# Optimization experiments

Hardware: AMD Instinct MI355X
Metric: run time of the kernel (lower is better)

Reference implementation:

```python
import jax, jax.numpy as jnp
import numpy as np

B, S, HID = 2, 2048, 2048
NH, NKV, HD = 16, 4, 128
GROUPS = NH // NKV
ROPE_BASE = 10000.0


def setup_inputs() -> dict:
    key = jax.random.key(0)
    ks = jax.random.split(key, 12)

    def w(k, i, o):
        return (jax.random.normal(k, (i, o), jnp.float32) * (i ** -0.5)).astype(jnp.float32)

    return {
        'x_real': jax.random.normal(ks[0], (B, S, HID), jnp.float32),
        'x_imag': jax.random.normal(ks[1], (B, S, HID), jnp.float32),
        'Wq_r': w(ks[2], HID, HID), 'Wq_i': w(ks[3], HID, HID),
        'bq_r': jnp.zeros((HID,), jnp.float32), 'bq_i': jnp.zeros((HID,), jnp.float32),
        'Wk_r': w(ks[4], HID, NKV * HD), 'Wk_i': w(ks[5], HID, NKV * HD),
        'bk_r': jnp.zeros((NKV * HD,), jnp.float32), 'bk_i': jnp.zeros((NKV * HD,), jnp.float32),
        'Wv_r': w(ks[6], HID, NKV * HD), 'Wv_i': w(ks[7], HID, NKV * HD),
        'bv_r': jnp.zeros((NKV * HD,), jnp.float32), 'bv_i': jnp.zeros((NKV * HD,), jnp.float32),
        'Wo_r': w(ks[8], HID, HID), 'Wo_i': w(ks[9], HID, HID),
        'bo_r': jnp.zeros((HID,), jnp.float32), 'bo_i': jnp.zeros((HID,), jnp.float32),
    }


def _clinear(xr, xi, Wr, Wi, br, bi):
    # complex linear: (xr + i*xi) @ (Wr + i*Wi) + (br + i*bi)
    out_r = xr @ Wr - xi @ Wi + br
    out_i = xr @ Wi + xi @ Wr + bi
    return out_r, out_i


def _split_heads(xr, xi, n_heads):
    b, s, _ = xr.shape
    xr = xr.reshape(b, s, n_heads, -1).transpose(0, 2, 1, 3)  # [B,H,S,D]
    xi = xi.reshape(b, s, n_heads, -1).transpose(0, 2, 1, 3)
    return xr, xi


def _rope(xr, xi):
    # complex rotary embedding: multiply (xr + i*xi) by exp(i * pos * inv_freq)
    s, d = xr.shape[-2], xr.shape[-1]
    inv_freq = 1.0 / (ROPE_BASE ** (jnp.arange(0, d, 2, dtype=jnp.float32) / d))
    freqs = jnp.arange(s, dtype=jnp.float32)[:, None] * inv_freq[None, :]  # [S, D/2]
    emb = jnp.concatenate([freqs, freqs], axis=-1)  # [S, D]
    cos, sin = jnp.cos(emb), jnp.sin(emb)
    return xr * cos - xi * sin, xr * sin + xi * cos


def _repeat_kv(xr, xi):
    if GROUPS == 1:
        return xr, xi
    b, hkv, s, d = xr.shape
    xr = jnp.broadcast_to(xr[:, :, None], (b, hkv, GROUPS, s, d)).reshape(b, NH, s, d)
    xi = jnp.broadcast_to(xi[:, :, None], (b, hkv, GROUPS, s, d)).reshape(b, NH, s, d)
    return xr, xi


def reference(x_real, x_imag, Wq_r, Wq_i, bq_r, bq_i, Wk_r, Wk_i, bk_r, bk_i,
              Wv_r, Wv_i, bv_r, bv_i, Wo_r, Wo_i, bo_r, bo_i):
    q_r, q_i = _clinear(x_real, x_imag, Wq_r, Wq_i, bq_r, bq_i)
    k_r, k_i = _clinear(x_real, x_imag, Wk_r, Wk_i, bk_r, bk_i)
    v_r, v_i = _clinear(x_real, x_imag, Wv_r, Wv_i, bv_r, bv_i)

    q_r, q_i = _split_heads(q_r, q_i, NH)
    k_r, k_i = _split_heads(k_r, k_i, NKV)
    v_r, v_i = _split_heads(v_r, v_i, NKV)

    q_r, q_i = _rope(q_r, q_i)
    k_r, k_i = _rope(k_r, k_i)

    k_r, k_i = _repeat_kv(k_r, k_i)
    v_r, v_i = _repeat_kv(v_r, v_i)

    scale = 1.0 / jnp.sqrt(jnp.float32(HD))
    # real part of complex inner product q . conj(k)
    scores = (jnp.einsum('bhqd,bhkd->bhqk', q_r, k_r)
              + jnp.einsum('bhqd,bhkd->bhqk', q_i, k_i)) * scale
    s = scores.shape[-1]
    causal = jnp.tril(jnp.ones((s, s), bool))
    scores = jnp.where(causal, scores, jnp.float32(-1e9))
    attn = jax.nn.softmax(scores, axis=-1)  # [B,H,S,S]

    out_r = jnp.einsum('bhqk,bhkd->bhqd', attn, v_r)
    out_i = jnp.einsum('bhqk,bhkd->bhqd', attn, v_i)

    # merge heads
    b = out_r.shape[0]
    out_r = out_r.transpose(0, 2, 1, 3).reshape(b, s, NH * HD)
    out_i = out_i.transpose(0, 2, 1, 3).reshape(b, s, NH * HD)

    out_r, out_i = _clinear(out_r, out_i, Wo_r, Wo_i, bo_r, bo_i)
    return out_r, out_i, attn
```

## Files before the change

kernel.cpp:

```cpp
#include <hip/hip_runtime.h>
#include <hip/hip_bf16.h>

#define S_LEN 2048
#define HIDDEN 2048
#define NHEAD 16
#define NKVH 4
#define HEADD 128
#define BATCH 2

typedef __attribute__((ext_vector_type(4))) float f32x4;
typedef __attribute__((ext_vector_type(8))) short bf16x8;
typedef __attribute__((ext_vector_type(4))) unsigned short u16x4;

__device__ __forceinline__ unsigned short f2bf(float f) {
  union { __hip_bfloat16 h; unsigned short u; } cv;
  cv.h = __float2bfloat16(f);
  return cv.u;
}

__device__ __forceinline__ float bf2f(unsigned short u) {
  union { float f; unsigned int i; } cv;
  cv.i = (unsigned int)u << 16;
  return cv.f;
}

__device__ __forceinline__ void gl_lds16(const void* g, void* l) {
  __builtin_amdgcn_global_load_lds(
      (const __attribute__((address_space(1))) unsigned int*)g,
      (__attribute__((address_space(3))) unsigned int*)l,
      16, 0, 0);
}

__device__ __forceinline__ f32x4 mfma16(bf16x8 a, bf16x8 b, f32x4 c) {
  return __builtin_amdgcn_mfma_f32_16x16x32_bf16(a, b, c, 0, 0, 0);
}

__global__ void k_rope_table(float* tab) {
  int idx = blockIdx.x * blockDim.x + threadIdx.x;
  if (idx >= S_LEN * 64) return;
  int s = idx >> 6, j = idx & 63;
  float invf = expf(-(float)j * (logf(10000.0f) / 64.0f));
  float ang = (float)s * invf;
  float sn, cs;
  sincosf(ang, &sn, &cs);
  tab[idx * 2 + 0] = cs;
  tab[idx * 2 + 1] = sn;
}

__global__ void k_pack_x(const float* __restrict__ xr, const float* __restrict__ xi,
                         unsigned short* __restrict__ Xp) {
  int idx = blockIdx.x * blockDim.x + threadIdx.x;
  if (idx >= 4096 * 4096 / 4) return;
  int m = idx >> 10;
  int c4 = idx & 1023;
  const float* src = (c4 < 512) ? (xr + (size_t)m * 2048 + c4 * 4)
                                : (xi + (size_t)m * 2048 + (c4 - 512) * 4);
  f32x4 v = *(const f32x4*)src;
  ((u16x4*)Xp)[idx] = (u16x4){f2bf(v.x), f2bf(v.y), f2bf(v.z), f2bf(v.w)};
}

__global__ void k_pack_w(const float* __restrict__ wq_r, const float* __restrict__ wq_i,
                         const float* __restrict__ wk_r, const float* __restrict__ wk_i,
                         const float* __restrict__ wv_r, const float* __restrict__ wv_i,
                         const float* __restrict__ wo_r, const float* __restrict__ wo_i,
                         unsigned short* __restrict__ Wt) {
  __shared__ float tile[32][33];
  int k0 = blockIdx.x * 32;
  int n0 = blockIdx.y * 32;
  int tx = threadIdx.x, ty0 = threadIdx.y;
#pragma unroll
  for (int i = 0; i < 4; ++i) {
    int ty = ty0 + i * 8;
    int k = k0 + ty;
    int n = n0 + tx;
    const float* Wr; const float* Wi; int w, part, j;
    if (n < 4096) {
      Wr = wq_r; Wi = wq_i; w = 2048;
      int h = n >> 8, p = (n >> 7) & 1, d = n & 127;
      part = p; j = h * 128 + d;
    } else if (n < 5120) {
      Wr = wk_r; Wi = wk_i; w = 512;
      int t = n - 4096;
      int kv = t >> 8, p = (t >> 7) & 1, d = t & 127;
      part = p; j = kv * 128 + d;
    } else if (n < 6144) {
      Wr = wv_r; Wi = wv_i; w = 512;
      int t = n - 5120;
      int kv = t >> 8, p = (t >> 7) & 1, d = t & 127;
      part = p; j = kv * 128 + d;
    } else {
      Wr = wo_r; Wi = wo_i; w = 2048;
      int t = n - 6144;
      part = (t >= w); j = part ? (t - w) : t;
    }
    float v;
    if (part == 0) v = (k < 2048) ? Wr[(size_t)k * w + j] : -Wi[(size_t)(k - 2048) * w + j];
    else           v = (k < 2048) ? Wi[(size_t)k * w + j] :  Wr[(size_t)(k - 2048) * w + j];
    tile[ty][tx] = v;
  }
  __syncthreads();
#pragma unroll
  for (int i = 0; i < 4; ++i) {
    int ty = ty0 + i * 8;
    Wt[(size_t)(n0 + ty) * 4096 + k0 + tx] = f2bf(tile[tx][ty]);
  }
}

template <int MODE>
__global__ __launch_bounds__(512, 2) void k_gemm256(
    const unsigned short* __restrict__ A, const unsigned short* __restrict__ Bt,
    int NTN,
    float* __restrict__ outR, float* __restrict__ outI,
    const float* __restrict__ bR, const float* __restrict__ bI,
    const float* __restrict__ tab,
    const float* __restrict__ bqr, const float* __restrict__ bqi,
    const float* __restrict__ bkr, const float* __restrict__ bki,
    const float* __restrict__ bvr, const float* __restrict__ bvi,
    unsigned short* __restrict__ Qcat, unsigned short* __restrict__ Kcat,
    unsigned short* __restrict__ VtP) {
  constexpr int KD = 4096;
  constexpr int Kb = KD * 2;
  constexpr int NT = KD / 64;
  constexpr int NITER = NT / 2;
  __shared__ __align__(16) char smem[131072];
  int tid = threadIdx.x, lane = tid & 63, wid = tid >> 6;
  int wm = wid >> 2, wn = wid & 3;
  int nwg = gridDim.x;
  int bid = blockIdx.x;
  int swz = (bid & 7) * (nwg >> 3) + (bid >> 3);
  int mt = swz / NTN, nt = swz - mt * NTN;
  int m0 = mt * 256, n0 = nt * 256;

  const char* Ab = (const char*)A + (size_t)m0 * Kb;
  const char* Bb = (const char*)Bt + (size_t)n0 * Kb;
  char* L = smem;

  int i0 = tid, i1 = tid + 512;
  int pl0 = (i0 >> 3) * Kb + (((i0 & 7) ^ ((i0 >> 3) & 7)) << 4);
  int pl1 = (i1 >> 3) * Kb + (((i1 & 7) ^ ((i1 >> 3) & 7)) << 4);

  int jx0 = (((lane >> 4)) ^ (lane & 7)) << 4;
  int jx1 = (((lane >> 4) + 4) ^ (lane & 7)) << 4;
  int arow = (wm * 64 + (lane & 15)) * 128;
  int brow = (wn * 32 + (lane & 15)) * 128;

  auto STAGE_A = [&](int buf, int half, int kt) {
    const char* s = Ab + (size_t)half * 128 * Kb + kt * 128;
    char* d = L + buf * 32768 + half * 16384 + (wid << 10);
    gl_lds16(s + pl0, d);
    gl_lds16(s + pl1, d + 8192);
  };
  auto STAGE_B = [&](int buf, int half, int kt) {
    const char* s = Bb + (size_t)half * 128 * Kb + kt * 128;
    char* d = L + 65536 + buf * 32768 + half * 16384 + (wid << 10);
    gl_lds16(s + pl0, d);
    gl_lds16(s + pl1, d + 8192);
  };
  auto LD_A = [&](bf16x8* dst, int buf, int half) {
    const char* base = L + buf * 32768 + half * 16384 + arow;
#pragma unroll
    for (int mf = 0; mf < 4; ++mf) {
      dst[mf * 2 + 0] = *(const bf16x8*)(base + mf * 2048 + jx0);
      dst[mf * 2 + 1] = *(const bf16x8*)(base + mf * 2048 + jx1);
    }
  };
  auto LD_B = [&](bf16x8* dst, int buf, int half) {
    const char* base = L + 65536 + buf * 32768 + half * 16384 + brow;
#pragma unroll
    for (int nf = 0; nf < 2; ++nf) {
      dst[nf * 2 + 0] = *(const bf16x8*)(base + nf * 2048 + jx0);
      dst[nf * 2 + 1] = *(const bf16x8*)(base + nf * 2048 + jx1);
    }
  };

  f32x4 acc[8][4];
  const f32x4 fz = {0.f, 0.f, 0.f, 0.f};
#pragma unroll
  for (int i = 0; i < 8; ++i)
#pragma unroll
    for (int j = 0; j < 4; ++j) acc[i][j] = fz;

  bf16x8 aX[8], aY[8], bX[4], bY[4];

#define BARR() __builtin_amdgcn_s_barrier()
#define WAITV(drain) do { if (drain) asm volatile("s_waitcnt vmcnt(0)" ::: "memory"); \
                          else       asm volatile("s_waitcnt vmcnt(6)" ::: "memory"); } while (0)
#define MMQ(aS, bS, qm, qn) do { \
    __builtin_amdgcn_s_setprio(1); \
    _Pragma("unroll") \
    for (int mf = 0; mf < 4; ++mf) \
      _Pragma("unroll") \
      for (int nf = 0; nf < 2; ++nf) { \
        acc[(qm)*4+mf][(qn)*2+nf] = mfma16(aS[mf*2+0], bS[nf*2+0], acc[(qm)*4+mf][(qn)*2+nf]); \
        acc[(qm)*4+mf][(qn)*2+nf] = mfma16(aS[mf*2+1], bS[nf*2+1], acc[(qm)*4+mf][(qn)*2+nf]); \
      } \
    __builtin_amdgcn_s_setprio(0); \
  } while (0)

  STAGE_A(0, 0, 0);
  STAGE_B(0, 0, 0);
  STAGE_B(0, 1, 0);
  STAGE_A(0, 1, 0);
  STAGE_A(1, 0, 1);
  STAGE_B(1, 0, 1);
  STAGE_B(1, 1, 1);
  asm volatile("s_waitcnt vmcnt(6)" ::: "memory");
  BARR();

  for (int it = 0; it < NITER; ++it) {
    int t1 = 2 * it + 1, t2 = 2 * it + 2, t3 = 2 * it + 3;
    bool nl = (it < NITER - 1);
    LD_A(aX, 0, 0); LD_B(bX, 0, 0);
    STAGE_A(1, 1, t1);
    BARR(); MMQ(aX, bX, 0, 0); BARR();
    LD_B(bY, 0, 1);
    if (nl) STAGE_A(0, 0, t2);
    BARR(); MMQ(aX, bY, 0, 1); BARR();
    LD_A(aY, 0, 1);
    if (nl) STAGE_B(0, 0, t2);
    BARR(); MMQ(aY, bY, 1, 1); BARR();
    if (nl) STAGE_B(0, 1, t2);
    WAITV(!nl); BARR(); MMQ(aY, bX, 1, 0); BARR();
    LD_A(aX, 1, 0); LD_B(bY, 1, 0);
    if (nl) STAGE_A(0, 1, t2);
    BARR(); MMQ(aX, bY, 0, 0); BARR();
    LD_B(bX, 1, 1);
    if (nl) STAGE_A(1, 0, t3);
    BARR(); MMQ(aX, bX, 0, 1); BARR();
    LD_A(aY, 1, 1);
    if (nl) STAGE_B(1, 0, t3);
    BARR(); MMQ(aY, bX, 1, 1); BARR();
    if (nl) STAGE_B(1, 1, t3);
    WAITV(!nl); BARR(); MMQ(aY, bY, 1, 0); BARR();
  }

  int r0 = (lane >> 4) << 2, col0 = lane & 15;

  if (MODE == 1) {
#pragma unroll
    for (int qm = 0; qm < 2; ++qm)
#pragma unroll
      for (int mf = 0; mf < 4; ++mf)
#pragma unroll
        for (int qn = 0; qn < 2; ++qn)
#pragma unroll
          for (int nf = 0; nf < 2; ++nf) {
            f32x4 v = acc[qm * 4 + mf][qn * 2 + nf];
            int rowb = m0 + qm * 128 + wm * 64 + mf * 16 + r0;
            int col = n0 + qn * 128 + wn * 32 + nf * 16 + col0;
#pragma unroll
            for (int r = 0; r < 4; ++r) {
              int row = rowb + r;
              if (col < 2048) outR[(size_t)row * 2048 + col] = v[r] + bR[col];
              else            outI[(size_t)row * 2048 + (col - 2048)] = v[r] + bI[col - 2048];
            }
          }
    return;
  }

  __syncthreads();
  int bidx = m0 >> 11;
  int s0 = m0 & 2047;

  if (n0 < 5120) {
    bool isQ = (n0 < 4096);
    int hh = isQ ? (n0 >> 8) : ((n0 - 4096) >> 8);
    const float* bRp = isQ ? bqr : bkr;
    const float* bIp = isQ ? bqi : bki;
    int jbase = hh * 128;
#pragma unroll
    for (int qm = 0; qm < 2; ++qm)
#pragma unroll
      for (int mf = 0; mf < 4; ++mf)
#pragma unroll
        for (int nf = 0; nf < 2; ++nf) {
          int d = wn * 32 + nf * 16 + col0;
          f32x4 vr = acc[qm * 4 + mf][0 * 2 + nf];
          f32x4 vi = acc[qm * 4 + mf][1 * 2 + nf];
          float br = bRp[jbase + d], bi = bIp[jbase + d];
#pragma unroll
          for (int r = 0; r < 4; ++r) {
            int lrow = qm * 128 + wm * 64 + mf * 16 + r0 + r;
            int s = s0 + lrow;
            float2 cs = *(const float2*)(tab + ((size_t)s * 64 + (d & 63)) * 2);
            float qr = vr[r] + br;
            float qi = vi[r] + bi;
            float orr = qr * cs.x - qi * cs.y;
            float oii = qr * cs.y + qi * cs.x;
            int swz4 = (lrow & 3) << 3;
            int g0 = (d >> 3) ^ swz4;
            int g1 = ((128 + d) >> 3) ^ swz4;
            *(unsigned short*)(L + lrow * 512 + g0 * 16 + (d & 7) * 2) = f2bf(orr);
            *(unsigned short*)(L + lrow * 512 + g1 * 16 + (d & 7) * 2) = f2bf(oii);
          }
        }
    __syncthreads();
    char* dstb = isQ ? (char*)Qcat + ((size_t)(bidx * 16 + hh) * 2048 + s0) * 512
                     : (char*)Kcat + ((size_t)(bidx * 4 + hh) * 2048 + s0) * 512;
#pragma unroll
    for (int i = 0; i < 16; ++i) {
      int cid = tid + 512 * i;
      int row = cid >> 5, c = cid & 31;
      int g = c ^ ((row & 3) << 3);
      *(f32x4*)(dstb + (size_t)row * 512 + c * 16) = *(const f32x4*)(L + row * 512 + g * 16);
    }
  } else {
    int kv = (n0 - 5120) >> 8;
#pragma unroll
    for (int qm = 0; qm < 2; ++qm)
#pragma unroll
      for (int mf = 0; mf < 4; ++mf)
#pragma unroll
        for (int qn = 0; qn < 2; ++qn)
#pragma unroll
          for (int nf = 0; nf < 2; ++nf) {
            int dloc = wn * 32 + nf * 16 + col0;
            int nlocal = qn * 128 + dloc;
            f32x4 v = acc[qm * 4 + mf][qn * 2 + nf];
            float bias = (qn ? bvi : bvr)[kv * 128 + dloc];
#pragma unroll
            for (int r = 0; r < 4; ++r) {
              int lrow = qm * 128 + wm * 64 + mf * 16 + r0 + r;
              int g = (lrow >> 3) ^ (nlocal & 31);
              *(unsigned short*)(L + nlocal * 512 + g * 16 + (lrow & 7) * 2) =
                  f2bf(v[r] + bias);
            }
          }
    __syncthreads();
    char* dstb = (char*)VtP + (size_t)(bidx * 4 + kv) * 256 * 4096 + (size_t)s0 * 2;
#pragma unroll
    for (int i = 0; i < 16; ++i) {
      int cid = tid + 512 * i;
      int n = cid >> 5, c = cid & 31;
      int g = c ^ (n & 31);
      *(f32x4*)(dstb + (size_t)n * 4096 + c * 16) = *(const f32x4*)(L + n * 512 + g * 16);
    }
  }
#undef BARR
#undef WAITV
#undef MMQ
}

__global__ __launch_bounds__(512, 4) void k_attn_fused(
    const unsigned short* __restrict__ Qcat, const unsigned short* __restrict__ Kcat,
    const unsigned short* __restrict__ Vt, float* __restrict__ attn,
    unsigned short* __restrict__ Cpack) {
  __shared__ __align__(16) char smem[74240];
  const float scale = 0.08838834764831845f;
  const float SH = 16.0f;

  int tid = threadIdx.x, lane = tid & 63, wid = tid >> 6;
  int l15 = lane & 15, l4 = lane >> 4;
  int bid = blockIdx.x;
  int qt = 31 - (bid >> 5), bh = bid & 31;
  int b = bh >> 4, h = bh & 15;
  int nt = qt + 1;

  const char* Qb = (const char*)Qcat + (size_t)bh * S_LEN * 512 + (size_t)qt * 64 * 512;
  const char* Kb = (const char*)Kcat + (size_t)(b * NKVH + (h >> 2)) * S_LEN * 512;
  const char* Vb = (const char*)Vt + (size_t)(b * NKVH + (h >> 2)) * 256 * (size_t)S_LEN * 2;
  float* P = attn + (size_t)bh * S_LEN * S_LEN;

  int r5 = tid >> 5, c5 = tid & 31;
  int sw512 = ((c5 ^ (r5 & 7)) << 4);
  int r3 = tid >> 3, c3 = tid & 7;
  int sw128 = ((c3 ^ (r3 & 7)) << 4);
  char* ldst = smem + (wid << 10);

  auto stQ = [&]() {
#pragma unroll
    for (int c = 0; c < 4; ++c)
      gl_lds16(Qb + (size_t)(c * 16 + r5) * 512 + sw512, ldst + c * 8192);
  };
  auto stK = [&](int base, int kv0) {
#pragma unroll
    for (int c = 0; c < 4; ++c)
      gl_lds16(Kb + (size_t)(kv0 + c * 16 + r5) * 512 + sw512, ldst + base + c * 8192);
  };
  auto stV = [&](int kv0) {
#pragma unroll
    for (int c = 0; c < 4; ++c)
      gl_lds16(Vb + (size_t)(c * 64 + r3) * 4096 + kv0 * 2 + sw128,
               ldst + 32768 + c * 8192);
  };

  float* sPart = (float*)(smem + 65536);
  float* sML = (float*)(smem + 73728);

#define BARL() do { asm volatile("s_waitcnt lgkmcnt(0)" ::: "memory"); \
                    __builtin_amdgcn_s_barrier(); } while (0)

  stQ();
  asm volatile("s_waitcnt vmcnt(0)" ::: "memory");
  __builtin_amdgcn_s_barrier();
  bf16x8 q[8];
  {
    int row = (wid >> 1) * 16 + l15;
#pragma unroll
    for (int kf = 0; kf < 8; ++kf)
      q[kf] = *(const bf16x8*)(smem + row * 512 + (((kf * 4 + l4) ^ (row & 7)) << 4));
  }
  BARL();

  auto QKT = [&](f32x4 accs[2], int kbase) {
#pragma unroll
    for (int kf = 0; kf < 8; ++kf) {
      bf16x8 bb[2];
#pragma unroll
      for (int nf = 0; nf < 2; ++nf) {
        int row = (wid & 1) * 32 + nf * 16 + l15;
        bb[nf] = *(const bf16x8*)(smem + kbase + row * 512 +
                                  (((kf * 4 + l4) ^ (row & 7)) << 4));
      }
      accs[0] = mfma16(q[kf], bb[0], accs[0]);
      accs[1] = mfma16(q[kf], bb[1], accs[1]);
    }
  };

  stK(0, 0);
  stK(32768, 64);
  asm volatile("s_waitcnt vmcnt(4)" ::: "memory");
  __builtin_amdgcn_s_barrier();

  float lacc[4] = {0.f, 0.f, 0.f, 0.f};
  for (int t = 0; t < nt; ++t) {
    int kbase = (t & 1) * 32768;
    f32x4 accs[2];
    accs[0] = (f32x4){0.f, 0.f, 0.f, 0.f};
    accs[1] = (f32x4){0.f, 0.f, 0.f, 0.f};
    QKT(accs, kbase);
    BARL();
    if (t + 2 < nt) stK(kbase, (t + 2) * 64);
    int kv0 = t * 64;
#pragma unroll
    for (int r = 0; r < 4; ++r) {
      int lrow = (wid >> 1) * 16 + l4 * 4 + r;
      int grow = qt * 64 + lrow;
      int cA = kv0 + (wid & 1) * 32 + l15;
      float e0 = (cA <= grow) ? __expf(accs[0][r] * scale - SH) : 0.f;
      float e1 = (cA + 16 <= grow) ? __expf(accs[1][r] * scale - SH) : 0.f;
      lacc[r] += e0 + e1;
    }
    if (t + 1 < nt) {
      if (t + 2 < nt) asm volatile("s_waitcnt vmcnt(4)" ::: "memory");
      else            asm volatile("s_waitcnt vmcnt(0)" ::: "memory");
      __builtin_amdgcn_s_barrier();
    }
  }
#pragma unroll
  for (int r = 0; r < 4; ++r) {
#pragma unroll
    for (int o = 1; o < 16; o <<= 1) lacc[r] += __shfl_xor(lacc[r], o);
  }
  if (l15 == 0) {
#pragma unroll
    for (int r = 0; r < 4; ++r) {
      int lrow = (wid >> 1) * 16 + l4 * 4 + r;
      sPart[(wid & 1) * 64 + lrow] = lacc[r];
    }
  }
  BARL();
  if (tid < 64) sML[tid] = 1.0f / (sPart[tid] + sPart[64 + tid]);
  asm volatile("s_waitcnt vmcnt(0) lgkmcnt(0)" ::: "memory");
  __builtin_amdgcn_s_barrier();

  stK(0, 0);
  stV(0);
  asm volatile("s_waitcnt vmcnt(0)" ::: "memory");
  __builtin_amdgcn_s_barrier();

  int wmP = wid >> 2, wnP = wid & 3;
  f32x4 accp[2][4];
#pragma unroll
  for (int i = 0; i < 2; ++i)
#pragma unroll
    for (int j = 0; j < 4; ++j) accp[i][j] = (f32x4){0.f, 0.f, 0.f, 0.f};

  for (int t = 0; t < nt; ++t) {
    bool more = (t + 1 < nt);
    f32x4 accs[2];
    accs[0] = (f32x4){0.f, 0.f, 0.f, 0.f};
    accs[1] = (f32x4){0.f, 0.f, 0.f, 0.f};
    QKT(accs, 0);
    BARL();
    if (more) stK(0, (t + 1) * 64);
    int kv0 = t * 64;
#pragma unroll
    for (int r = 0; r < 4; ++r) {
      int lrow = (wid >> 1) * 16 + l4 * 4 + r;
      int grow = qt * 64 + lrow;
      float mi = sML[lrow];
#pragma unroll
      for (int nf = 0; nf < 2; ++nf) {
        int lcol = (wid & 1) * 32 + nf * 16 + l15;
        int gcol = kv0 + lcol;
        float s = accs[nf][r] * scale;
        float p = (gcol <= grow) ? __expf(s - SH) * mi : 0.f;
        *(unsigned short*)(smem + 65536 + lrow * 128 +
                           (((lcol >> 3) ^ (lrow & 7)) << 4) + (lcol & 7) * 2) = f2bf(p);
      }
    }
    asm volatile("s_waitcnt lgkmcnt(0)" ::: "memory");
    if (more) asm volatile("s_waitcnt vmcnt(4)" ::: "memory");
    else      asm volatile("s_waitcnt vmcnt(0)" ::: "memory");
    __builtin_amdgcn_s_barrier();
#pragma unroll
    for (int p = 0; p < 2; ++p) {
      int idx = tid + 512 * p;
      int row = idx >> 4, c16 = idx & 15;
      int byte = 65536 + row * 128 + (((c16 >> 1) ^ (row & 7)) << 4) + (c16 & 1) * 8;
      u16x4 pv = *(const u16x4*)(smem + byte);
      f32x4 o = {bf2f(pv.x), bf2f(pv.y), bf2f(pv.z), bf2f(pv.w)};
      *(f32x4*)(P + (size_t)(qt * 64 + row) * S_LEN + kv0 + c16 * 4) = o;
    }
    __builtin_amdgcn_s_setprio(1);
#pragma unroll
    for (int ks = 0; ks < 2; ++ks) {
      bf16x8 a[2], bb[4];
#pragma unroll
      for (int mf = 0; mf < 2; ++mf) {
        int row = wmP * 32 + mf * 16 + l15;
        a[mf] = *(const bf16x8*)(smem + 65536 + row * 128 +
                                 (((ks * 4 + l4) ^ (row & 7)) << 4));
      }
#pragma unroll
      for (int nf = 0; nf < 4; ++nf) {
        int n = wnP * 64 + nf * 16 + l15;
        bb[nf] = *(const bf16x8*)(smem + 32768 + n * 128 +
                                  (((ks * 4 + l4) ^ (n & 7)) << 4));
      }
#pragma unroll
      for (int mf = 0; mf < 2; ++mf)
#pragma unroll
        for (int nf = 0; nf < 4; ++nf)
          accp[mf][nf] = mfma16(a[mf], bb[nf], accp[mf][nf]);
    }
    __builtin_amdgcn_s_setprio(0);
    BARL();
    if (more) {
      stV((t + 1) * 64);
      asm volatile("s_waitcnt vmcnt(6)" ::: "memory");
    }
    __builtin_amdgcn_s_barrier();
  }

  {
    int c0 = 64 * (qt + 1);
    const f32x4 z4 = {0.f, 0.f, 0.f, 0.f};
    for (int rr = 0; rr < 8; ++rr) {
      int grow = qt * 64 + wid * 8 + rr;
      for (int c = c0 + lane * 4; c < 2048; c += 256)
        *(f32x4*)(P + (size_t)grow * S_LEN + c) = z4;
    }
  }
  int r0w = l4 * 4;
#pragma unroll
  for (int mf = 0; mf < 2; ++mf)
#pragma unroll
    for (int nf = 0; nf < 4; ++nf) {
      int gmb = qt * 64 + wmP * 32 + mf * 16 + r0w;
      int nn = wnP * 64 + nf * 16 + l15;
      int gcol = (nn < 128) ? (h * 128 + nn) : (2048 + h * 128 + (nn - 128));
#pragma unroll
      for (int r = 0; r < 4; ++r)
        Cpack[(size_t)(b * S_LEN + gmb + r) * 4096 + gcol] = f2bf(accp[mf][nf][r]);
    }
#undef BARL
}

extern "C" void kernel_launch(void* const* d_in, const int* in_sizes, int n_in,
                              void* d_out, int out_size, void* d_ws, size_t ws_size,
                              hipStream_t stream) {
  const float* xr = (const float*)d_in[0];
  const float* xi = (const float*)d_in[1];
  const float* wq_r = (const float*)d_in[2];
  const float* wq_i = (const float*)d_in[3];
  const float* bq_r = (const float*)d_in[4];
  const float* bq_i = (const float*)d_in[5];
  const float* wk_r = (const float*)d_in[6];
  const float* wk_i = (const float*)d_in[7];
  const float* bk_r = (const float*)d_in[8];
  const float* bk_i = (const float*)d_in[9];
  const float* wv_r = (const float*)d_in[10];
  const float* wv_i = (const float*)d_in[11];
  const float* bv_r = (const float*)d_in[12];
  const float* bv_i = (const float*)d_in[13];
  const float* wo_r = (const float*)d_in[14];
  const float* wo_i = (const float*)d_in[15];
  const float* bo_r = (const float*)d_in[16];
  const float* bo_i = (const float*)d_in[17];

  float* out = (float*)d_out;
  float* outR = out;
  float* outI = out + (size_t)BATCH * S_LEN * HIDDEN;
  float* attn = outI + (size_t)BATCH * S_LEN * HIDDEN;

  char* ws = (char*)d_ws;
  size_t off = 0;
  auto alloc = [&](size_t bytes) {
    char* p = ws + off;
    off += (bytes + 255) & ~(size_t)255;
    return p;
  };
  unsigned short* Xp = (unsigned short*)alloc((size_t)4096 * 4096 * 2);
  unsigned short* Wt = (unsigned short*)alloc((size_t)10240 * 4096 * 2);
  float* tab = (float*)alloc((size_t)S_LEN * 64 * 2 * 4);
  unsigned short* Qcat = (unsigned short*)alloc((size_t)BATCH * NHEAD * S_LEN * 256 * 2);
  unsigned short* Kcat = (unsigned short*)alloc((size_t)BATCH * NKVH * S_LEN * 256 * 2);
  unsigned short* Vt = (unsigned short*)alloc((size_t)BATCH * NKVH * 256 * S_LEN * 2);
  unsigned short* Cpack = Xp;

  k_rope_table<<<512, 256, 0, stream>>>(tab);
  k_pack_x<<<16384, 256, 0, stream>>>(xr, xi, Xp);
  k_pack_w<<<dim3(128, 320), dim3(32, 8), 0, stream>>>(wq_r, wq_i, wk_r, wk_i, wv_r, wv_i,
                                                       wo_r, wo_i, Wt);
  k_gemm256<2><<<384, 512, 0, stream>>>(Xp, Wt, 24,
                                        nullptr, nullptr, nullptr, nullptr,
                                        tab, bq_r, bq_i, bk_r, bk_i, bv_r, bv_i,
                                        Qcat, Kcat, Vt);
  k_attn_fused<<<1024, 512, 0, stream>>>(Qcat, Kcat, Vt, attn, Cpack);
  k_gemm256<1><<<256, 512, 0, stream>>>(Cpack, Wt + (size_t)6144 * 4096, 16,
                                        outR, outI, bo_r, bo_i,
                                        nullptr, nullptr, nullptr, nullptr, nullptr,
                                        nullptr, nullptr, nullptr, nullptr, nullptr);
}
```

Before: 724.7 us.

## Load Q/K/V fragments directly from global memory in attention kernel, double-buffer P

Removes the LDS staging of Q, K and V tiles (async global-to-LDS copies plus their waits and barriers) in the fused attention kernel. MFMA operands are now read straight from global memory, relying on the cache for reuse. The P tile is double-buffered in a much smaller LDS allocation, which lets one barrier per iteration go and may raise occupancy. The cost is uncoalesced, redundant global loads per wave and the loss of the explicit prefetch pipelining.

Result: slower. 1.098 ms (+51.5%).

```diff
diff --git a/kernel.cpp b/kernel.cpp
--- a/kernel.cpp
+++ b/kernel.cpp
@@ -345,7 +345,7 @@
     const unsigned short* __restrict__ Qcat, const unsigned short* __restrict__ Kcat,
     const unsigned short* __restrict__ Vt, float* __restrict__ attn,
     unsigned short* __restrict__ Cpack) {
-  __shared__ __align__(16) char smem[74240];
+  __shared__ __align__(16) char smem[17664];
   const float scale = 0.08838834764831845f;
   const float SH = 16.0f;
 
@@ -361,76 +361,38 @@
   const char* Vb = (const char*)Vt + (size_t)(b * NKVH + (h >> 2)) * 256 * (size_t)S_LEN * 2;
   float* P = attn + (size_t)bh * S_LEN * S_LEN;
 
-  int r5 = tid >> 5, c5 = tid & 31;
-  int sw512 = ((c5 ^ (r5 & 7)) << 4);
-  int r3 = tid >> 3, c3 = tid & 7;
-  int sw128 = ((c3 ^ (r3 & 7)) << 4);
-  char* ldst = smem + (wid << 10);
-
-  auto stQ = [&]() {
-#pragma unroll
-    for (int c = 0; c < 4; ++c)
-      gl_lds16(Qb + (size_t)(c * 16 + r5) * 512 + sw512, ldst + c * 8192);
-  };
-  auto stK = [&](int base, int kv0) {
-#pragma unroll
-    for (int c = 0; c < 4; ++c)
-      gl_lds16(Kb + (size_t)(kv0 + c * 16 + r5) * 512 + sw512, ldst + base + c * 8192);
-  };
-  auto stV = [&](int kv0) {
-#pragma unroll
-    for (int c = 0; c < 4; ++c)
-      gl_lds16(Vb + (size_t)(c * 64 + r3) * 4096 + kv0 * 2 + sw128,
-               ldst + 32768 + c * 8192);
-  };
-
-  float* sPart = (float*)(smem + 65536);
-  float* sML = (float*)(smem + 73728);
+  float* sPart = (float*)(smem + 16384);
+  float* sML = (float*)(smem + 16896);
 
 #define BARL() do { asm volatile("s_waitcnt lgkmcnt(0)" ::: "memory"); \
                     __builtin_amdgcn_s_barrier(); } while (0)
 
-  stQ();
-  asm volatile("s_waitcnt vmcnt(0)" ::: "memory");
-  __builtin_amdgcn_s_barrier();
   bf16x8 q[8];
   {
     int row = (wid >> 1) * 16 + l15;
 #pragma unroll
     for (int kf = 0; kf < 8; ++kf)
-      q[kf] = *(const bf16x8*)(smem + row * 512 + (((kf * 4 + l4) ^ (row & 7)) << 4));
-  }
-  BARL();
-
-  auto QKT = [&](f32x4 accs[2], int kbase) {
+      q[kf] = *(const bf16x8*)(Qb + (size_t)row * 512 + (kf * 4 + l4) * 16);
+  }
+
+  int krow0 = (wid & 1) * 32 + l15;
+  auto QKT = [&](f32x4 accs[2], int t) {
+    const char* kb = Kb + (size_t)(t * 64 + krow0) * 512 + l4 * 16;
 #pragma unroll
     for (int kf = 0; kf < 8; ++kf) {
-      bf16x8 bb[2];
-#pragma unroll
-      for (int nf = 0; nf < 2; ++nf) {
-        int row = (wid & 1) * 32 + nf * 16 + l15;
-        bb[nf] = *(const bf16x8*)(smem + kbase + row * 512 +
-                                  (((kf * 4 + l4) ^ (row & 7)) << 4));
-      }
-      accs[0] = mfma16(q[kf], bb[0], accs[0]);
-      accs[1] = mfma16(q[kf], bb[1], accs[1]);
+      bf16x8 b0 = *(const bf16x8*)(kb + kf * 64);
+      bf16x8 b1 = *(const bf16x8*)(kb + 16 * 512 + kf * 64);
+      accs[0] = mfma16(q[kf], b0, accs[0]);
+      accs[1] = mfma16(q[kf], b1, accs[1]);
     }
   };
-
-  stK(0, 0);
-  stK(32768, 64);
-  asm volatile("s_waitcnt vmcnt(4)" ::: "memory");
-  __builtin_amdgcn_s_barrier();
 
   float lacc[4] = {0.f, 0.f, 0.f, 0.f};
   for (int t = 0; t < nt; ++t) {
-    int kbase = (t & 1) * 32768;
     f32x4 accs[2];
     accs[0] = (f32x4){0.f, 0.f, 0.f, 0.f};
     accs[1] = (f32x4){0.f, 0.f, 0.f, 0.f};
-    QKT(accs, kbase);
-    BARL();
-    if (t + 2 < nt) stK(kbase, (t + 2) * 64);
+    QKT(accs, t);
     int kv0 = t * 64;
 #pragma unroll
     for (int r = 0; r < 4; ++r) {
@@ -441,11 +403,6 @@
       float e1 = (cA + 16 <= grow) ? __expf(accs[1][r] * scale - SH) : 0.f;
       lacc[r] += e0 + e1;
     }
-    if (t + 1 < nt) {
-      if (t + 2 < nt) asm volatile("s_waitcnt vmcnt(4)" ::: "memory");
-      else            asm volatile("s_waitcnt vmcnt(0)" ::: "memory");
-      __builtin_amdgcn_s_barrier();
-    }
   }
 #pragma unroll
   for (int r = 0; r < 4; ++r) {
@@ -461,15 +418,10 @@
   }
   BARL();
   if (tid < 64) sML[tid] = 1.0f / (sPart[tid] + sPart[64 + tid]);
-  asm volatile("s_waitcnt vmcnt(0) lgkmcnt(0)" ::: "memory");
-  __builtin_amdgcn_s_barrier();
-
-  stK(0, 0);
-  stV(0);
-  asm volatile("s_waitcnt vmcnt(0)" ::: "memory");
-  __builtin_amdgcn_s_barrier();
+  BARL();
 
   int wmP = wid >> 2, wnP = wid & 3;
+  int vrow0 = wnP * 64 + l15;
   f32x4 accp[2][4];
 #pragma unroll
   for (int i = 0; i < 2; ++i)
@@ -477,13 +429,11 @@
     for (int j = 0; j < 4; ++j) accp[i][j] = (f32x4){0.f, 0.f, 0.f, 0.f};
 
   for (int t = 0; t < nt; ++t) {
-    bool more = (t + 1 < nt);
+    char* sPb = smem + (t & 1) * 8192;
     f32x4 accs[2];
     accs[0] = (f32x4){0.f, 0.f, 0.f, 0.f};
     accs[1] = (f32x4){0.f, 0.f, 0.f, 0.f};
-    QKT(accs, 0);
-    BARL();
-    if (more) stK(0, (t + 1) * 64);
+    QKT(accs, t);
     int kv0 = t * 64;
 #pragma unroll
     for (int r = 0; r < 4; ++r) {
@@ -496,20 +446,17 @@
         int gcol = kv0 + lcol;
         float s = accs[nf][r] * scale;
         float p = (gcol <= grow) ? __expf(s - SH) * mi : 0.f;
-        *(unsigned short*)(smem + 65536 + lrow * 128 +
+        *(unsigned short*)(sPb + lrow * 128 +
                            (((lcol >> 3) ^ (lrow & 7)) << 4) + (lcol & 7) * 2) = f2bf(p);
       }
     }
-    asm volatile("s_waitcnt lgkmcnt(0)" ::: "memory");
-    if (more) asm volatile("s_waitcnt vmcnt(4)" ::: "memory");
-    else      asm volatile("s_waitcnt vmcnt(0)" ::: "memory");
-    __builtin_amdgcn_s_barrier();
+    BARL();
 #pragma unroll
     for (int p = 0; p < 2; ++p) {
       int idx = tid + 512 * p;
       int row = idx >> 4, c16 = idx & 15;
-      int byte = 65536 + row * 128 + (((c16 >> 1) ^ (row & 7)) << 4) + (c16 & 1) * 8;
-      u16x4 pv = *(const u16x4*)(smem + byte);
+      int byte = row * 128 + (((c16 >> 1) ^ (row & 7)) << 4) + (c16 & 1) * 8;
+      u16x4 pv = *(const u16x4*)(sPb + byte);
       f32x4 o = {bf2f(pv.x), bf2f(pv.y), bf2f(pv.z), bf2f(pv.w)};
       *(f32x4*)(P + (size_t)(qt * 64 + row) * S_LEN + kv0 + c16 * 4) = o;
     }
@@ -520,14 +467,12 @@
 #pragma unroll
       for (int mf = 0; mf < 2; ++mf) {
         int row = wmP * 32 + mf * 16 + l15;
-        a[mf] = *(const bf16x8*)(smem + 65536 + row * 128 +
-                                 (((ks * 4 + l4) ^ (row & 7)) << 4));
+        a[mf] = *(const bf16x8*)(sPb + row * 128 + (((ks * 4 + l4) ^ (row & 7)) << 4));
       }
 #pragma unroll
       for (int nf = 0; nf < 4; ++nf) {
-        int n = wnP * 64 + nf * 16 + l15;
-        bb[nf] = *(const bf16x8*)(smem + 32768 + n * 128 +
-                                  (((ks * 4 + l4) ^ (n & 7)) << 4));
+        int n = vrow0 + nf * 16;
+        bb[nf] = *(const bf16x8*)(Vb + (size_t)n * 4096 + t * 128 + ks * 64 + l4 * 16);
       }
 #pragma unroll
       for (int mf = 0; mf < 2; ++mf)
@@ -536,12 +481,6 @@
           accp[mf][nf] = mfma16(a[mf], bb[nf], accp[mf][nf]);
     }
     __builtin_amdgcn_s_setprio(0);
-    BARL();
-    if (more) {
-      stV((t + 1) * 64);
-      asm volatile("s_waitcnt vmcnt(6)" ::: "memory");
-    }
-    __builtin_amdgcn_s_barrier();
   }
 
   {
```

## Drop the row-sum pre-pass and normalize attention output and probabilities afterward

Applied to the files above, without the earlier changes.

Removes the first QK^T pass that only computed the softmax denominators. The remaining single pass now accumulates row sums alongside the unnormalized exponentials used in the PV matmul. The output accumulator is scaled by the inverse sum at the end, and the inverse sums are written to a workspace. A new k_pnorm kernel then rereads the stored attention rows, rescales them and writes the upper triangle as zeros. This trades a recomputation of QK^T for an extra read-modify-write pass over the large attention probability tensor.

After: 799.8 us. +10.4%, slower.

```diff
diff --git a/kernel.cpp b/kernel.cpp
--- a/kernel.cpp
+++ b/kernel.cpp
@@ -344,7 +344,7 @@
 __global__ __launch_bounds__(512, 4) void k_attn_fused(
     const unsigned short* __restrict__ Qcat, const unsigned short* __restrict__ Kcat,
     const unsigned short* __restrict__ Vt, float* __restrict__ attn,
-    unsigned short* __restrict__ Cpack) {
+    unsigned short* __restrict__ Cpack, float* __restrict__ minv) {
   __shared__ __align__(16) char smem[74240];
   const float scale = 0.08838834764831845f;
   const float SH = 16.0f;
@@ -418,53 +418,6 @@
   };
 
   stK(0, 0);
-  stK(32768, 64);
-  asm volatile("s_waitcnt vmcnt(4)" ::: "memory");
-  __builtin_amdgcn_s_barrier();
-
-  float lacc[4] = {0.f, 0.f, 0.f, 0.f};
-  for (int t = 0; t < nt; ++t) {
-    int kbase = (t & 1) * 32768;
-    f32x4 accs[2];
-    accs[0] = (f32x4){0.f, 0.f, 0.f, 0.f};
-    accs[1] = (f32x4){0.f, 0.f, 0.f, 0.f};
-    QKT(accs, kbase);
-    BARL();
-    if (t + 2 < nt) stK(kbase, (t + 2) * 64);
-    int kv0 = t * 64;
-#pragma unroll
-    for (int r = 0; r < 4; ++r) {
-      int lrow = (wid >> 1) * 16 + l4 * 4 + r;
-      int grow = qt * 64 + lrow;
-      int cA = kv0 + (wid & 1) * 32 + l15;
-      float e0 = (cA <= grow) ? __expf(accs[0][r] * scale - SH) : 0.f;
-      float e1 = (cA + 16 <= grow) ? __expf(accs[1][r] * scale - SH) : 0.f;
-      lacc[r] += e0 + e1;
-    }
-    if (t + 1 < nt) {
-      if (t + 2 < nt) asm volatile("s_waitcnt vmcnt(4)" ::: "memory");
-      else            asm volatile("s_waitcnt vmcnt(0)" ::: "memory");
-      __builtin_amdgcn_s_barrier();
-    }
-  }
-#pragma unroll
-  for (int r = 0; r < 4; ++r) {
-#pragma unroll
-    for (int o = 1; o < 16; o <<= 1) lacc[r] += __shfl_xor(lacc[r], o);
-  }
-  if (l15 == 0) {
-#pragma unroll
-    for (int r = 0; r < 4; ++r) {
-      int lrow = (wid >> 1) * 16 + l4 * 4 + r;
-      sPart[(wid & 1) * 64 + lrow] = lacc[r];
-    }
-  }
-  BARL();
-  if (tid < 64) sML[tid] = 1.0f / (sPart[tid] + sPart[64 + tid]);
-  asm volatile("s_waitcnt vmcnt(0) lgkmcnt(0)" ::: "memory");
-  __builtin_amdgcn_s_barrier();
-
-  stK(0, 0);
   stV(0);
   asm volatile("s_waitcnt vmcnt(0)" ::: "memory");
   __builtin_amdgcn_s_barrier();
@@ -475,6 +428,7 @@
   for (int i = 0; i < 2; ++i)
 #pragma unroll
     for (int j = 0; j < 4; ++j) accp[i][j] = (f32x4){0.f, 0.f, 0.f, 0.f};
+  float lacc[4] = {0.f, 0.f, 0.f, 0.f};
 
   for (int t = 0; t < nt; ++t) {
     bool more = (t + 1 < nt);
@@ -489,15 +443,15 @@
     for (int r = 0; r < 4; ++r) {
       int lrow = (wid >> 1) * 16 + l4 * 4 + r;
       int grow = qt * 64 + lrow;
-      float mi = sML[lrow];
 #pragma unroll
       for (int nf = 0; nf < 2; ++nf) {
         int lcol = (wid & 1) * 32 + nf * 16 + l15;
         int gcol = kv0 + lcol;
         float s = accs[nf][r] * scale;
-        float p = (gcol <= grow) ? __expf(s - SH) * mi : 0.f;
+        float e = (gcol <= grow) ? __expf(s - SH) : 0.f;
+        lacc[r] += e;
         *(unsigned short*)(smem + 65536 + lrow * 128 +
-                           (((lcol >> 3) ^ (lrow & 7)) << 4) + (lcol & 7) * 2) = f2bf(p);
+                           (((lcol >> 3) ^ (lrow & 7)) << 4) + (lcol & 7) * 2) = f2bf(e);
       }
     }
     asm volatile("s_waitcnt lgkmcnt(0)" ::: "memory");
@@ -544,16 +498,36 @@
     __builtin_amdgcn_s_barrier();
   }
 
-  {
-    int c0 = 64 * (qt + 1);
-    const f32x4 z4 = {0.f, 0.f, 0.f, 0.f};
-    for (int rr = 0; rr < 8; ++rr) {
-      int grow = qt * 64 + wid * 8 + rr;
-      for (int c = c0 + lane * 4; c < 2048; c += 256)
-        *(f32x4*)(P + (size_t)grow * S_LEN + c) = z4;
-    }
-  }
+#pragma unroll
+  for (int r = 0; r < 4; ++r) {
+#pragma unroll
+    for (int o = 1; o < 16; o <<= 1) lacc[r] += __shfl_xor(lacc[r], o);
+  }
+  if (l15 == 0) {
+#pragma unroll
+    for (int r = 0; r < 4; ++r) {
+      int lrow = (wid >> 1) * 16 + l4 * 4 + r;
+      sPart[(wid & 1) * 64 + lrow] = lacc[r];
+    }
+  }
+  BARL();
+  if (tid < 64) {
+    float iv = 1.0f / (sPart[tid] + sPart[64 + tid]);
+    sML[tid] = iv;
+    minv[(size_t)bh * S_LEN + qt * 64 + tid] = iv;
+  }
+  BARL();
+
   int r0w = l4 * 4;
+#pragma unroll
+  for (int mf = 0; mf < 2; ++mf) {
+#pragma unroll
+    for (int r = 0; r < 4; ++r) {
+      float iv = sML[wmP * 32 + mf * 16 + r0w + r];
+#pragma unroll
+      for (int nf = 0; nf < 4; ++nf) accp[mf][nf][r] *= iv;
+    }
+  }
 #pragma unroll
   for (int mf = 0; mf < 2; ++mf)
 #pragma unroll
@@ -566,6 +540,34 @@
         Cpack[(size_t)(b * S_LEN + gmb + r) * 4096 + gcol] = f2bf(accp[mf][nf][r]);
     }
 #undef BARL
+}
+
+__global__ __launch_bounds__(256) void k_pnorm(float* __restrict__ attn,
+                                               const float* __restrict__ minv) {
+  int bh = blockIdx.y;
+  int row = blockIdx.x * 2 + (threadIdx.x >> 7);
+  int cbase = (threadIdx.x & 127) * 4;
+  float iv = minv[(size_t)bh * S_LEN + row];
+  float* pr = attn + ((size_t)bh * S_LEN + row) * S_LEN;
+  int q = row;
+#pragma unroll
+  for (int it = 0; it < 4; ++it) {
+    int c = cbase + it * 512;
+    f32x4 v;
+    if (c + 3 <= q) {
+      v = *(const f32x4*)(pr + c);
+      v.x *= iv; v.y *= iv; v.z *= iv; v.w *= iv;
+    } else if (c > q) {
+      v = (f32x4){0.f, 0.f, 0.f, 0.f};
+    } else {
+      v = *(const f32x4*)(pr + c);
+      v.x = (c + 0 <= q) ? v.x * iv : 0.f;
+      v.y = (c + 1 <= q) ? v.y * iv : 0.f;
+      v.z = (c + 2 <= q) ? v.z * iv : 0.f;
+      v.w = (c + 3 <= q) ? v.w * iv : 0.f;
+    }
+    *(f32x4*)(pr + c) = v;
+  }
 }
 
 extern "C" void kernel_launch(void* const* d_in, const int* in_sizes, int n_in,
@@ -608,6 +610,7 @@
   unsigned short* Qcat = (unsigned short*)alloc((size_t)BATCH * NHEAD * S_LEN * 256 * 2);
   unsigned short* Kcat = (unsigned short*)alloc((size_t)BATCH * NKVH * S_LEN * 256 * 2);
   unsigned short* Vt = (unsigned short*)alloc((size_t)BATCH * NKVH * 256 * S_LEN * 2);
+  float* minv = (float*)alloc((size_t)32 * S_LEN * 4);
   unsigned short* Cpack = Xp;
 
   k_rope_table<<<512, 256, 0, stream>>>(tab);
@@ -618,7 +621,8 @@
                                         nullptr, nullptr, nullptr, nullptr,
                                         tab, bq_r, bq_i, bk_r, bk_i, bv_r, bv_i,
                                         Qcat, Kcat, Vt);
-  k_attn_fused<<<1024, 512, 0, stream>>>(Qcat, Kcat, Vt, attn, Cpack);
+  k_attn_fused<<<1024, 512, 0, stream>>>(Qcat, Kcat, Vt, attn, Cpack, minv);
+  k_pnorm<<<dim3(1024, 32), 256, 0, stream>>>(attn, minv);
   k_gemm256<1><<<256, 512, 0, stream>>>(Cpack, Wt + (size_t)6144 * 4096, 16,
                                         outR, outI, bo_r, bo_i,
                                         nullptr, nullptr, nullptr, nullptr, nullptr,
```
